# Kernel tuning notes

Hardware: AMD Instinct MI355X
Metric: run time of the kernel (lower is better)

The kernel has to match this reference:

```python
import jax, jax.numpy as jnp
import numpy as np

B, N, D = 2, 2048, 1024
H = 16
HS = D // H
EPS = 1e-6


def layer_norm(x, scale, bias):
    mu = jnp.mean(x, axis=-1, keepdims=True)
    var = jnp.mean(jnp.square(x - mu), axis=-1, keepdims=True)
    return (x - mu) * jax.lax.rsqrt(var + EPS) * scale + bias


def setup_inputs() -> dict:
    key = jax.random.key(0)
    ks = jax.random.split(key, 8)
    lecun = lambda k, shape: jax.random.normal(k, shape, jnp.float32) / jnp.sqrt(shape[0])
    return {
        "x": jax.random.normal(ks[0], (B, N, D), jnp.float32),
        "ln1_scale": jnp.ones((D,), jnp.float32),
        "ln1_bias": jnp.zeros((D,), jnp.float32),
        "w_qkv": lecun(ks[1], (D, 3 * D)),
        "w_out": lecun(ks[2], (D, D)),
        "b_out": jnp.zeros((D,), jnp.float32),
        "ln2_scale": jnp.ones((D,), jnp.float32),
        "ln2_bias": jnp.zeros((D,), jnp.float32),
        "w1": lecun(ks[3], (D, 2 * D)),
        "b1": jnp.zeros((2 * D,), jnp.float32),
        "w2": lecun(ks[4], (2 * D, D)),
        "b2": jnp.zeros((D,), jnp.float32),
    }


def reference(x, ln1_scale, ln1_bias, w_qkv, w_out, b_out,
              ln2_scale, ln2_bias, w1, b1, w2, b2):
    b, n, d = x.shape
    # --- attention sub-block ---
    xn = layer_norm(x, ln1_scale, ln1_bias)
    qkv = xn @ w_qkv                      # [B,N,3D]
    q, k, v = jnp.split(qkv, 3, axis=-1)
    q = q.reshape(b, n, H, HS)
    k = k.reshape(b, n, H, HS)
    v = v.reshape(b, n, H, HS)
    scores = jnp.einsum('bihd,bjhd->bhij', q, k) / jnp.sqrt(jnp.float32(HS))
    causal = jnp.tril(jnp.ones((n, n), bool))[None, None]
    scores = jnp.where(causal, scores, -jnp.inf)
    attn = jax.nn.softmax(scores, axis=-1)
    out_heads = jnp.einsum('bhij,bjhd->bihd', attn, v).reshape(b, n, d)
    x = x + out_heads @ w_out + b_out
    xn2 = layer_norm(x, ln2_scale, ln2_bias)
    y = jax.nn.gelu(xn2 @ w1 + b1)        # flax nn.gelu default approximate=True
    x = x + (y @ w2 + b2)
    return x
```

## Files before the change

### kernel.cpp

```cpp
#include <hip/hip_runtime.h>

#define D_MODEL 1024
#define NSEQ    2048
#define NBATCH  2
#define NHEAD   16
#define HSZ     64
#define MROWS   4096

typedef short s8v  __attribute__((ext_vector_type(8)));
typedef short s4v  __attribute__((ext_vector_type(4)));
typedef float f32x4 __attribute__((ext_vector_type(4)));
typedef float f32x16 __attribute__((ext_vector_type(16)));

#define AS1(p) ((__attribute__((address_space(1))) const void*)(p))
#define AS3(p) ((__attribute__((address_space(3))) void*)(p))

__device__ __forceinline__ float b2f(unsigned short s) {
    union { unsigned u; float f; } z; z.u = (unsigned)s << 16; return z.f;
}
__device__ __forceinline__ unsigned short f2b(float f) {
    union { float f; unsigned u; } z; z.f = f;
    unsigned r = z.u + 0x7fffu + ((z.u >> 16) & 1u);
    return (unsigned short)(r >> 16);
}
__device__ __forceinline__ unsigned short f2b_trunc(float f) {
    union { float f; unsigned u; } z; z.f = f;
    return (unsigned short)(z.u >> 16);
}
__device__ __forceinline__ float gelu_f(float x) {
    float u = 0.7978845608028654f * (x + 0.044715f * x * x * x);
    float t = 1.f - 2.f / (1.f + __expf(2.f * u));
    return 0.5f * x * (1.f + t);
}
__device__ __forceinline__ unsigned cvt_pk_bf16(float lo, float hi) {
    unsigned r;
    asm("v_cvt_pk_bf16_f32 %0, %1, %2" : "=v"(r) : "v"(lo), "v"(hi));
    return r;
}

__global__ __launch_bounds__(256) void sniff_k(const unsigned short* __restrict__ xr,
                                               int* __restrict__ flag) {
    __shared__ int cnt[4];
    int tid = threadIdx.x, ok = 0;
    for (int i = tid; i < 2048; i += 256) {
        unsigned short u = xr[i];
        int e = (u >> 7) & 0xFF;
        if (u == 0 || (e >= 110 && e <= 135)) ok++;
    }
    #pragma unroll
    for (int off = 32; off; off >>= 1) ok += __shfl_down(ok, off);
    if ((tid & 63) == 0) cnt[tid >> 6] = ok;
    __syncthreads();
    if (tid == 0) {
        int tot = cnt[0] + cnt[1] + cnt[2] + cnt[3];
        *flag = (tot > 1843) ? 1 : 0;
    }
}

__global__ __launch_bounds__(256) void cvt_small_k(
    const void* p0, const void* p1, const void* p2, const void* p3,
    const void* p4, const void* p5, const void* p6,
    unsigned short* __restrict__ out, const int* __restrict__ flag)
{
    int i = blockIdx.x * 256 + threadIdx.x;
    const void* src; int off;
    if      (i < 1024) { src = p0; off = i; }
    else if (i < 2048) { src = p1; off = i - 1024; }
    else if (i < 3072) { src = p2; off = i - 2048; }
    else if (i < 4096) { src = p3; off = i - 3072; }
    else if (i < 5120) { src = p4; off = i - 4096; }
    else if (i < 7168) { src = p5; off = i - 5120; }
    else               { src = p6; off = i - 7168; }
    out[i] = (*flag) ? ((const unsigned short*)src)[off]
                     : f2b(((const float*)src)[off]);
}

__global__ __launch_bounds__(256) void transpose_all_k(
    const void* wqkv, const void* wout, const void* w1, const void* w2,
    unsigned short* t_qkv, unsigned short* t_out,
    unsigned short* t_w1, unsigned short* t_w2, const int* __restrict__ flag)
{
    __shared__ unsigned short t[32][33];
    int bid = blockIdx.x;
    const void* W; unsigned short* Wt; int K, N, bx, by;
    if      (bid < 3072) { W = wqkv; Wt = t_qkv; K = 1024; N = 3072; bx = bid % 96; by = bid / 96; }
    else if (bid < 4096) { bid -= 3072; W = wout; Wt = t_out; K = 1024; N = 1024; bx = bid % 32; by = bid / 32; }
    else if (bid < 6144) { bid -= 4096; W = w1;   Wt = t_w1;  K = 1024; N = 2048; bx = bid % 64; by = bid / 64; }
    else                 { bid -= 6144; W = w2;   Wt = t_w2;  K = 2048; N = 1024; bx = bid % 32; by = bid / 32; }
    int f = *flag;
    int n0 = bx * 32, k0 = by * 32;
    int x = threadIdx.x & 31, y = threadIdx.x >> 5;
    #pragma unroll
    for (int r = 0; r < 32; r += 8) {
        size_t idx = (size_t)(k0 + r + y) * N + n0 + x;
        t[r + y][x] = f ? ((const unsigned short*)W)[idx]
                        : f2b(((const float*)W)[idx]);
    }
    __syncthreads();
    #pragma unroll
    for (int r = 0; r < 32; r += 8)
        Wt[(size_t)(n0 + r + y) * K + k0 + x] = t[x][r + y];
}

__global__ __launch_bounds__(256) void ln1f_k(
    const void* __restrict__ x_raw, const unsigned short* __restrict__ scale,
    const unsigned short* __restrict__ bias, unsigned short* __restrict__ xb,
    unsigned short* __restrict__ xn, const int* __restrict__ flag)
{
    int row = blockIdx.x, tid = threadIdx.x;
    int f = *flag;
    float v[4], s = 0.f, s2 = 0.f;
    #pragma unroll
    for (int i = 0; i < 4; ++i) {
        size_t idx = (size_t)row * D_MODEL + tid + i * 256;
        float t = f ? b2f(((const unsigned short*)x_raw)[idx])
                    : ((const float*)x_raw)[idx];
        v[i] = t; s += t; s2 += t * t;
    }
    #pragma unroll
    for (int off = 32; off; off >>= 1) { s += __shfl_down(s, off); s2 += __shfl_down(s2, off); }
    __shared__ float rs[4], rs2[4];
    int w = tid >> 6;
    if ((tid & 63) == 0) { rs[w] = s; rs2[w] = s2; }
    __syncthreads();
    float S  = rs[0] + rs[1] + rs[2] + rs[3];
    float S2 = rs2[0] + rs2[1] + rs2[2] + rs2[3];
    float mean = S * (1.f / D_MODEL);
    float var  = S2 * (1.f / D_MODEL) - mean * mean;
    float rstd = rsqrtf(var + 1e-6f);
    #pragma unroll
    for (int i = 0; i < 4; ++i) {
        int d = tid + i * 256;
        size_t idx = (size_t)row * D_MODEL + d;
        xb[idx] = f2b(v[i]);
        xn[idx] = f2b((v[i] - mean) * rstd * b2f(scale[d]) + b2f(bias[d]));
    }
}

__global__ __launch_bounds__(256) void ln_k(
    const unsigned short* __restrict__ x, const unsigned short* __restrict__ scale,
    const unsigned short* __restrict__ bias, unsigned short* __restrict__ out)
{
    int row = blockIdx.x, tid = threadIdx.x;
    const unsigned short* xr = x + (size_t)row * D_MODEL;
    float v[4], s = 0.f, s2 = 0.f;
    #pragma unroll
    for (int i = 0; i < 4; ++i) {
        float t = b2f(xr[tid + i * 256]);
        v[i] = t; s += t; s2 += t * t;
    }
    #pragma unroll
    for (int off = 32; off; off >>= 1) { s += __shfl_down(s, off); s2 += __shfl_down(s2, off); }
    __shared__ float rs[4], rs2[4];
    int w = tid >> 6;
    if ((tid & 63) == 0) { rs[w] = s; rs2[w] = s2; }
    __syncthreads();
    float S  = rs[0] + rs[1] + rs[2] + rs[3];
    float S2 = rs2[0] + rs2[1] + rs2[2] + rs2[3];
    float mean = S * (1.f / D_MODEL);
    float var  = S2 * (1.f / D_MODEL) - mean * mean;
    float rstd = rsqrtf(var + 1e-6f);
    #pragma unroll
    for (int i = 0; i < 4; ++i) {
        int d = tid + i * 256;
        out[(size_t)row * D_MODEL + d] =
            f2b((v[i] - mean) * rstd * b2f(scale[d]) + b2f(bias[d]));
    }
}

template<int TN, int ACT, int RES, int ODYN>
__global__ __launch_bounds__(256) void gemm128_k(
    const unsigned short* __restrict__ A, const unsigned short* __restrict__ Bt,
    const unsigned short* __restrict__ bias, const unsigned short* __restrict__ resid,
    void* __restrict__ Cp, int M, int Nn, int K, const int* __restrict__ flag)
{
    constexpr int MT = (TN == 128) ? 4 : 2;
    __shared__ short As[128 * 64];
    __shared__ short Bs[TN * 64];
    int tid = threadIdx.x;
    int m0 = blockIdx.y * 128, n0 = blockIdx.x * TN;
    int lane = tid & 63, w = tid >> 6;
    int a_base = (TN == 128) ? (w >> 1) * 64 : w * 32;
    int b_base = (TN == 128) ? (w & 1) * 64 : 0;
    int mm = lane & 15, q = lane >> 4;

    f32x4 zero = {0.f, 0.f, 0.f, 0.f};
    f32x4 acc[MT][4];
    #pragma unroll
    for (int mt = 0; mt < MT; ++mt)
        #pragma unroll
        for (int nt = 0; nt < 4; ++nt) acc[mt][nt] = zero;

    int grow   = lane >> 3;
    int gchunk = ((lane & 7) ^ grow) * 8;
    const unsigned short* Ab = A  + (size_t)(m0 + w * 32 + grow) * K + gchunk;
    const unsigned short* Bb = Bt + (size_t)(n0 + w * (TN / 4) + grow) * K + gchunk;
    int swz = (mm & 7);

    for (int k0 = 0; k0 < K; k0 += 64) {
        __syncthreads();
        #pragma unroll
        for (int s = 0; s < 4; ++s)
            __builtin_amdgcn_global_load_lds(AS1(Ab + k0 + (size_t)(s * 8) * K),
                                             AS3(&As[(w * 32 + s * 8) * 64]), 16, 0, 0);
        #pragma unroll
        for (int s = 0; s < TN / 32; ++s)
            __builtin_amdgcn_global_load_lds(AS1(Bb + k0 + (size_t)(s * 8) * K),
                                             AS3(&Bs[(w * (TN / 4) + s * 8) * 64]), 16, 0, 0);
        __syncthreads();
        #pragma unroll
        for (int kk = 0; kk < 2; ++kk) {
            int col = ((kk * 4 + q) ^ swz) * 8;
            s8v af[MT], bf[4];
            #pragma unroll
            for (int mt = 0; mt < MT; ++mt)
                af[mt] = *(const s8v*)&As[(a_base + mt * 16 + mm) * 64 + col];
            #pragma unroll
            for (int nt = 0; nt < 4; ++nt)
                bf[nt] = *(const s8v*)&Bs[(b_base + nt * 16 + mm) * 64 + col];
            #pragma unroll
            for (int mt = 0; mt < MT; ++mt)
                #pragma unroll
                for (int nt = 0; nt < 4; ++nt)
                    acc[mt][nt] = __builtin_amdgcn_mfma_f32_16x16x32_bf16(
                        af[mt], bf[nt], acc[mt][nt], 0, 0, 0);
        }
    }

    int f = ODYN ? *flag : 1;
    #pragma unroll
    for (int nt = 0; nt < 4; ++nt) {
        int gc = n0 + b_base + nt * 16 + mm;
        float bv = bias ? b2f(bias[gc]) : 0.f;
        #pragma unroll
        for (int mt = 0; mt < MT; ++mt) {
            #pragma unroll
            for (int r = 0; r < 4; ++r) {
                int gr = m0 + a_base + mt * 16 + q * 4 + r;
                float v = acc[mt][nt][r] + bv;
                if (ACT == 1) v = gelu_f(v);
                if (RES == 1) v += b2f(resid[(size_t)gr * Nn + gc]);
                if (f) ((unsigned short*)Cp)[(size_t)gr * Nn + gc] = f2b(v);
                else   ((float*)Cp)[(size_t)gr * Nn + gc] = v;
            }
        }
    }
}

#define SWZG(r) ((((r) >> 3) ^ (r)) & 7)

__global__ __launch_bounds__(256, 4) void fattn_k(
    const unsigned short* __restrict__ qkv, unsigned short* __restrict__ attn_out)
{
    int bh = blockIdx.x;
    int h = bh & (NHEAD - 1), b = bh >> 4;
    int qt = gridDim.y - 1 - blockIdx.y;
    int q0 = qt * 128;
    size_t base = (size_t)b * NSEQ * (3 * D_MODEL);

    __shared__ __align__(16) short Ks[64 * 64];
    __shared__ __align__(16) short Vt[64 * 64];

    int tid = threadIdx.x, lane = tid & 63, w = tid >> 6;
    int ql = lane & 31, hi = lane >> 5;
    int qw0 = q0 + w * 32;
    int gq = qw0 + ql;

    s8v qB[4];
    {
        const unsigned short* qrow = qkv + base + (size_t)gq * (3 * D_MODEL) + h * HSZ;
        #pragma unroll
        for (int ks = 0; ks < 4; ++ks) {
            s8v v = *(const s8v*)(qrow + ks * 16 + hi * 8);
            #pragma unroll
            for (int e = 0; e < 8; ++e) {
                unsigned short u = (unsigned short)v[e];
                if (u & 0x7f80u) u = (unsigned short)(u - 0x0180u);
                v[e] = (short)u;
            }
            qB[ks] = v;
        }
    }

    const unsigned short* kbase = qkv + base + D_MODEL + h * HSZ;
    const unsigned short* vbase = qkv + base + 2 * D_MODEL + h * HSZ;

    int krow = tid >> 2;
    int kc16 = (tid & 3) * 16;
    int km0  = (tid & 3) * 2;
    int kws0 = krow * 64 + (((km0    ) ^ SWZG(krow)) << 3);
    int kws1 = krow * 64 + (((km0 + 1) ^ SWZG(krow)) << 3);
    int kp = tid >> 3;
    int vd = (tid & 7) * 8;

    f32x16 z16;
    #pragma unroll
    for (int i = 0; i < 16; ++i) z16[i] = 0.f;
    f32x16 accA = z16, accB = z16;
    float l_acc = 0.f;

    int nstages = 2 * qt + 2;

    s8v ka, kb, va, vb;
    {
        const unsigned short* kr_ = kbase + (size_t)krow * (3 * D_MODEL) + kc16;
        ka = *(const s8v*)kr_;
        kb = *(const s8v*)(kr_ + 8);
        const unsigned short* vr_ = vbase + (size_t)(2 * kp) * (3 * D_MODEL) + vd;
        va = *(const s8v*)vr_;
        vb = *(const s8v*)(vr_ + 3 * D_MODEL);
    }

    for (int t = 0; t < nstages; ++t) {
        int j0 = t * 64;
        __syncthreads();
        *(s8v*)&Ks[kws0] = ka;
        *(s8v*)&Ks[kws1] = kb;
        #pragma unroll
        for (int e = 0; e < 8; ++e) {
            unsigned pv = (unsigned)(unsigned short)va[e] |
                          ((unsigned)(unsigned short)vb[e] << 16);
            int idx = (vd + e) * 64 + ((((kp >> 2) ^ (tid & 7) ^ e) & 7) << 3)
                      + ((2 * kp) & 7);
            *(unsigned*)&Vt[idx] = pv;
        }
        if (t + 1 < nstages) {
            const unsigned short* kr_ = kbase + (size_t)(j0 + 64 + krow) * (3 * D_MODEL) + kc16;
            ka = *(const s8v*)kr_;
            kb = *(const s8v*)(kr_ + 8);
            const unsigned short* vr_ = vbase + (size_t)(j0 + 64 + 2 * kp) * (3 * D_MODEL) + vd;
            va = *(const s8v*)vr_;
            vb = *(const s8v*)(vr_ + 3 * D_MODEL);
        }
        __syncthreads();

        if (j0 > qw0 + 31) continue;
        int nkt = (j0 + 32 <= qw0 + 31) ? 2 : 1;
        #pragma unroll
        for (int kt = 0; kt < 2; ++kt) {
            if (kt >= nkt) break;
            f32x16 sc = z16;
            __builtin_amdgcn_s_setprio(1);
            #pragma unroll
            for (int ks = 0; ks < 4; ++ks) {
                int key = kt * 32 + ql;
                s8v kf = *(const s8v*)&Ks[key * 64 + (((2 * ks + hi) ^ SWZG(key)) << 3)];
                sc = __builtin_amdgcn_mfma_f32_32x32x16_bf16(kf, qB[ks], sc, 0, 0, 0);
            }
            __builtin_amdgcn_s_setprio(0);
            bool needmask = (j0 + kt * 32 + 31) > qw0;
            #pragma unroll
            for (int r = 0; r < 16; ++r) {
                float p = __expf(sc[r]);
                if (needmask) {
                    int gk = j0 + kt * 32 + (r & 3) + 8 * (r >> 2) + 4 * hi;
                    if (gk > gq) p = 0.f;
                }
                l_acc += p;
                sc[r] = p;
            }
            #pragma unroll
            for (int slot = 0; slot < 2; ++slot) {
                union { unsigned u[4]; s8v v; } pu;
                pu.u[0] = cvt_pk_bf16(sc[slot * 8 + 0], sc[slot * 8 + 1]);
                pu.u[1] = cvt_pk_bf16(sc[slot * 8 + 2], sc[slot * 8 + 3]);
                pu.u[2] = cvt_pk_bf16(sc[slot * 8 + 4], sc[slot * 8 + 5]);
                pu.u[3] = cvt_pk_bf16(sc[slot * 8 + 6], sc[slot * 8 + 7]);
                int g1 = 4 * kt + 2 * slot;
                __builtin_amdgcn_s_setprio(1);
                #pragma unroll
                for (int dt = 0; dt < 2; ++dt) {
                    int dim = dt * 32 + ql;
                    int sw = SWZG(dim);
                    union { s4v hh[2]; s8v v; } vu;
                    vu.hh[0] = *(const s4v*)&Vt[dim * 64 + (((g1    ) ^ sw) << 3) + 4 * hi];
                    vu.hh[1] = *(const s4v*)&Vt[dim * 64 + (((g1 + 1) ^ sw) << 3) + 4 * hi];
                    if (dt == 0)
                        accA = __builtin_amdgcn_mfma_f32_32x32x16_bf16(pu.v, vu.v, accA, 0, 0, 0);
                    else
                        accB = __builtin_amdgcn_mfma_f32_32x32x16_bf16(pu.v, vu.v, accB, 0, 0, 0);
                }
                __builtin_amdgcn_s_setprio(0);
            }
        }
    }

    l_acc += __shfl_xor(l_acc, 32);
    float linv = 1.f / l_acc;
    unsigned short* orow = attn_out + (size_t)b * NSEQ * D_MODEL + h * HSZ;
    #pragma unroll
    for (int r = 0; r < 16; ++r) {
        int cr = (r & 3) + 8 * (r >> 2) + 4 * hi;
        float ri = __shfl(linv, cr);
        size_t ro = (size_t)(qw0 + cr) * D_MODEL;
        orow[ro + ql]      = f2b(accA[r] * ri);
        orow[ro + 32 + ql] = f2b(accB[r] * ri);
    }
}

extern "C" void kernel_launch(void* const* d_in, const int* in_sizes, int n_in,
                              void* d_out, int out_size, void* d_ws, size_t ws_size,
                              hipStream_t stream)
{
    const void* x_raw  = d_in[0];
    const void* ln1s_r = d_in[1];
    const void* ln1b_r = d_in[2];
    const void* wqkv_r = d_in[3];
    const void* wout_r = d_in[4];
    const void* bout_r = d_in[5];
    const void* ln2s_r = d_in[6];
    const void* ln2b_r = d_in[7];
    const void* w1_r   = d_in[8];
    const void* b1_r   = d_in[9];
    const void* w2_r   = d_in[10];
    const void* b2_r   = d_in[11];

    char* ws = (char*)d_ws;
    const size_t MB = 1024 * 1024;
    unsigned short* wt_qkv = (unsigned short*)(ws + 0 * MB);
    unsigned short* wt_out = (unsigned short*)(ws + 6 * MB);
    unsigned short* wt_w1  = (unsigned short*)(ws + 8 * MB);
    unsigned short* wt_w2  = (unsigned short*)(ws + 12 * MB);
    unsigned short* xb     = (unsigned short*)(ws + 16 * MB);
    unsigned short* xn     = (unsigned short*)(ws + 24 * MB);
    unsigned short* qkvb   = (unsigned short*)(ws + 32 * MB);
    unsigned short* x1     = (unsigned short*)(ws + 48 * MB);
    int*            flag   = (int*)           (ws + 56 * MB);
    unsigned short* cbias  = (unsigned short*)(ws + 56 * MB + 1024);
    unsigned short* attnb  = xn;
    unsigned short* xn2    = xn;
    unsigned short* hb     = qkvb;

    unsigned short* c_ln1s = cbias + 0;
    unsigned short* c_ln1b = cbias + 1024;
    unsigned short* c_bout = cbias + 2048;
    unsigned short* c_ln2s = cbias + 3072;
    unsigned short* c_ln2b = cbias + 4096;
    unsigned short* c_b1   = cbias + 5120;
    unsigned short* c_b2   = cbias + 7168;

    sniff_k<<<1, 256, 0, stream>>>((const unsigned short*)x_raw, flag);
    cvt_small_k<<<32, 256, 0, stream>>>(ln1s_r, ln1b_r, bout_r, ln2s_r, ln2b_r,
                                        b1_r, b2_r, cbias, flag);
    transpose_all_k<<<8192, 256, 0, stream>>>(wqkv_r, wout_r, w1_r, w2_r,
                                              wt_qkv, wt_out, wt_w1, wt_w2, flag);
    ln1f_k<<<MROWS, 256, 0, stream>>>(x_raw, c_ln1s, c_ln1b, xb, xn, flag);
    gemm128_k<128, 0, 0, 0><<<dim3(24, 32), 256, 0, stream>>>(
        xn, wt_qkv, nullptr, nullptr, qkvb, MROWS, 3072, 1024, flag);
    fattn_k<<<dim3(NBATCH * NHEAD, NSEQ / 128), 256, 0, stream>>>(qkvb, attnb);
    gemm128_k<64, 0, 1, 0><<<dim3(16, 32), 256, 0, stream>>>(
        attnb, wt_out, c_bout, xb, x1, MROWS, 1024, 1024, flag);
    ln_k<<<MROWS, 256, 0, stream>>>(x1, c_ln2s, c_ln2b, xn2);
    gemm128_k<128, 1, 0, 0><<<dim3(16, 32), 256, 0, stream>>>(
        xn2, wt_w1, c_b1, nullptr, hb, MROWS, 2048, 1024, flag);
    gemm128_k<64, 0, 1, 1><<<dim3(16, 32), 256, 0, stream>>>(
        hb, wt_w2, c_b2, x1, d_out, MROWS, 1024, 2048, flag);
}
```

Measured before the change: 297.2 us.

## Split attention KV range across two wave groups with 64-row query tiles

The attention kernel now uses 64-query tiles, doubling the grid. The block's four waves form two groups that each take alternate 64-key stages, with separate K/V shared buffers. Partial accumulators and row sums are merged through shared memory before normalisation. This is meant to raise parallelism and shorten the longest causal blocks, at the cost of a reduction step, extra shared memory, and per-group global-load imbalance.

```diff
diff --git a/kernel.cpp b/kernel.cpp
--- a/kernel.cpp
+++ b/kernel.cpp
@@ -11,6 +11,7 @@
 typedef short s4v  __attribute__((ext_vector_type(4)));
 typedef float f32x4 __attribute__((ext_vector_type(4)));
 typedef float f32x16 __attribute__((ext_vector_type(16)));
+typedef unsigned long long u64;
 
 #define AS1(p) ((__attribute__((address_space(1))) const void*)(p))
 #define AS3(p) ((__attribute__((address_space(3))) void*)(p))
@@ -22,10 +23,6 @@
     union { float f; unsigned u; } z; z.f = f;
     unsigned r = z.u + 0x7fffu + ((z.u >> 16) & 1u);
     return (unsigned short)(r >> 16);
-}
-__device__ __forceinline__ unsigned short f2b_trunc(float f) {
-    union { float f; unsigned u; } z; z.f = f;
-    return (unsigned short)(z.u >> 16);
 }
 __device__ __forceinline__ float gelu_f(float x) {
     float u = 0.7978845608028654f * (x + 0.044715f * x * x * x);
@@ -255,15 +252,17 @@
     int bh = blockIdx.x;
     int h = bh & (NHEAD - 1), b = bh >> 4;
     int qt = gridDim.y - 1 - blockIdx.y;
-    int q0 = qt * 128;
+    int q0 = qt * 64;
     size_t base = (size_t)b * NSEQ * (3 * D_MODEL);
 
-    __shared__ __align__(16) short Ks[64 * 64];
-    __shared__ __align__(16) short Vt[64 * 64];
-
+    __shared__ __align__(16) short smem[16384];
     int tid = threadIdx.x, lane = tid & 63, w = tid >> 6;
+    int g = w >> 1, wg = w & 1;
+    short* Ksg = &smem[g * 4096];
+    short* Vtg = &smem[8192 + g * 4096];
+
     int ql = lane & 31, hi = lane >> 5;
-    int qw0 = q0 + w * 32;
+    int qw0 = q0 + wg * 32;
     int gq = qw0 + ql;
 
     s8v qB[4];
@@ -285,13 +284,15 @@
     const unsigned short* kbase = qkv + base + D_MODEL + h * HSZ;
     const unsigned short* vbase = qkv + base + 2 * D_MODEL + h * HSZ;
 
-    int krow = tid >> 2;
-    int kc16 = (tid & 3) * 16;
-    int km0  = (tid & 3) * 2;
-    int kws0 = krow * 64 + (((km0    ) ^ SWZG(krow)) << 3);
-    int kws1 = krow * 64 + (((km0 + 1) ^ SWZG(krow)) << 3);
-    int kp = tid >> 3;
-    int vd = (tid & 7) * 8;
+    int tg = tid & 127;
+    int krow = tg >> 1;
+    int kc16 = (tg & 1) * 32;
+    int km0  = (tg & 1) * 4;
+    int swzk = SWZG(krow);
+    int kq  = tg >> 3;
+    int vd0 = (tg & 7) * 8;
+    int vslot = (kq & 1) * 4;
+    int vgg = kq >> 1;
 
     f32x16 z16;
     #pragma unroll
@@ -299,102 +300,137 @@
     f32x16 accA = z16, accB = z16;
     float l_acc = 0.f;
 
-    int nstages = 2 * qt + 2;
-
-    s8v ka, kb, va, vb;
-    {
-        const unsigned short* kr_ = kbase + (size_t)krow * (3 * D_MODEL) + kc16;
-        ka = *(const s8v*)kr_;
-        kb = *(const s8v*)(kr_ + 8);
-        const unsigned short* vr_ = vbase + (size_t)(2 * kp) * (3 * D_MODEL) + vd;
-        va = *(const s8v*)vr_;
-        vb = *(const s8v*)(vr_ + 3 * D_MODEL);
-    }
-
-    for (int t = 0; t < nstages; ++t) {
-        int j0 = t * 64;
+    int npairs = (qt + 2) >> 1;
+    int s = g;
+    bool valid = (s <= qt);
+
+    s8v ka0, ka1, ka2, ka3, va, vb, vc, vd_;
+    if (valid) {
+        const unsigned short* kr_ = kbase + (size_t)(s * 64 + krow) * (3 * D_MODEL) + kc16;
+        ka0 = *(const s8v*)kr_;
+        ka1 = *(const s8v*)(kr_ + 8);
+        ka2 = *(const s8v*)(kr_ + 16);
+        ka3 = *(const s8v*)(kr_ + 24);
+        const unsigned short* vr_ = vbase + (size_t)(s * 64 + 4 * kq) * (3 * D_MODEL) + vd0;
+        va  = *(const s8v*)vr_;
+        vb  = *(const s8v*)(vr_ + 3 * D_MODEL);
+        vc  = *(const s8v*)(vr_ + 6 * D_MODEL);
+        vd_ = *(const s8v*)(vr_ + 9 * D_MODEL);
+    }
+
+    for (int it = 0; it < npairs; ++it) {
+        int j0 = s * 64;
         __syncthreads();
-        *(s8v*)&Ks[kws0] = ka;
-        *(s8v*)&Ks[kws1] = kb;
-        #pragma unroll
-        for (int e = 0; e < 8; ++e) {
-            unsigned pv = (unsigned)(unsigned short)va[e] |
-                          ((unsigned)(unsigned short)vb[e] << 16);
-            int idx = (vd + e) * 64 + ((((kp >> 2) ^ (tid & 7) ^ e) & 7) << 3)
-                      + ((2 * kp) & 7);
-            *(unsigned*)&Vt[idx] = pv;
-        }
-        if (t + 1 < nstages) {
-            const unsigned short* kr_ = kbase + (size_t)(j0 + 64 + krow) * (3 * D_MODEL) + kc16;
-            ka = *(const s8v*)kr_;
-            kb = *(const s8v*)(kr_ + 8);
-            const unsigned short* vr_ = vbase + (size_t)(j0 + 64 + 2 * kp) * (3 * D_MODEL) + vd;
-            va = *(const s8v*)vr_;
-            vb = *(const s8v*)(vr_ + 3 * D_MODEL);
+        if (valid) {
+            *(s8v*)&Ksg[krow * 64 + (((km0 + 0) ^ swzk) << 3)] = ka0;
+            *(s8v*)&Ksg[krow * 64 + (((km0 + 1) ^ swzk) << 3)] = ka1;
+            *(s8v*)&Ksg[krow * 64 + (((km0 + 2) ^ swzk) << 3)] = ka2;
+            *(s8v*)&Ksg[krow * 64 + (((km0 + 3) ^ swzk) << 3)] = ka3;
+            #pragma unroll
+            for (int e = 0; e < 8; ++e) {
+                unsigned plo = (unsigned)(unsigned short)va[e] |
+                               ((unsigned)(unsigned short)vb[e] << 16);
+                unsigned phi = (unsigned)(unsigned short)vc[e] |
+                               ((unsigned)(unsigned short)vd_[e] << 16);
+                int dim = vd0 + e;
+                int col = ((vgg ^ (((tg & 7) ^ e) & 7)) << 3) + vslot;
+                *(u64*)&Vtg[dim * 64 + col] = (u64)plo | ((u64)phi << 32);
+            }
+        }
+        bool valid_n = (s + 2 <= qt);
+        if (valid_n) {
+            const unsigned short* kr_ = kbase + (size_t)((s + 2) * 64 + krow) * (3 * D_MODEL) + kc16;
+            ka0 = *(const s8v*)kr_;
+            ka1 = *(const s8v*)(kr_ + 8);
+            ka2 = *(const s8v*)(kr_ + 16);
+            ka3 = *(const s8v*)(kr_ + 24);
+            const unsigned short* vr_ = vbase + (size_t)((s + 2) * 64 + 4 * kq) * (3 * D_MODEL) + vd0;
+            va  = *(const s8v*)vr_;
+            vb  = *(const s8v*)(vr_ + 3 * D_MODEL);
+            vc  = *(const s8v*)(vr_ + 6 * D_MODEL);
+            vd_ = *(const s8v*)(vr_ + 9 * D_MODEL);
         }
         __syncthreads();
 
-        if (j0 > qw0 + 31) continue;
-        int nkt = (j0 + 32 <= qw0 + 31) ? 2 : 1;
-        #pragma unroll
-        for (int kt = 0; kt < 2; ++kt) {
-            if (kt >= nkt) break;
-            f32x16 sc = z16;
-            __builtin_amdgcn_s_setprio(1);
-            #pragma unroll
-            for (int ks = 0; ks < 4; ++ks) {
-                int key = kt * 32 + ql;
-                s8v kf = *(const s8v*)&Ks[key * 64 + (((2 * ks + hi) ^ SWZG(key)) << 3)];
-                sc = __builtin_amdgcn_mfma_f32_32x32x16_bf16(kf, qB[ks], sc, 0, 0, 0);
-            }
-            __builtin_amdgcn_s_setprio(0);
-            bool needmask = (j0 + kt * 32 + 31) > qw0;
-            #pragma unroll
-            for (int r = 0; r < 16; ++r) {
-                float p = __expf(sc[r]);
-                if (needmask) {
-                    int gk = j0 + kt * 32 + (r & 3) + 8 * (r >> 2) + 4 * hi;
-                    if (gk > gq) p = 0.f;
-                }
-                l_acc += p;
-                sc[r] = p;
-            }
-            #pragma unroll
-            for (int slot = 0; slot < 2; ++slot) {
-                union { unsigned u[4]; s8v v; } pu;
-                pu.u[0] = cvt_pk_bf16(sc[slot * 8 + 0], sc[slot * 8 + 1]);
-                pu.u[1] = cvt_pk_bf16(sc[slot * 8 + 2], sc[slot * 8 + 3]);
-                pu.u[2] = cvt_pk_bf16(sc[slot * 8 + 4], sc[slot * 8 + 5]);
-                pu.u[3] = cvt_pk_bf16(sc[slot * 8 + 6], sc[slot * 8 + 7]);
-                int g1 = 4 * kt + 2 * slot;
+        if (valid) {
+            int nkt = (j0 + 32 <= qw0 + 31) ? 2 : 1;
+            #pragma unroll
+            for (int kt = 0; kt < 2; ++kt) {
+                if (kt >= nkt) break;
+                f32x16 sc = z16;
                 __builtin_amdgcn_s_setprio(1);
                 #pragma unroll
-                for (int dt = 0; dt < 2; ++dt) {
-                    int dim = dt * 32 + ql;
-                    int sw = SWZG(dim);
-                    union { s4v hh[2]; s8v v; } vu;
-                    vu.hh[0] = *(const s4v*)&Vt[dim * 64 + (((g1    ) ^ sw) << 3) + 4 * hi];
-                    vu.hh[1] = *(const s4v*)&Vt[dim * 64 + (((g1 + 1) ^ sw) << 3) + 4 * hi];
-                    if (dt == 0)
-                        accA = __builtin_amdgcn_mfma_f32_32x32x16_bf16(pu.v, vu.v, accA, 0, 0, 0);
-                    else
-                        accB = __builtin_amdgcn_mfma_f32_32x32x16_bf16(pu.v, vu.v, accB, 0, 0, 0);
+                for (int ks = 0; ks < 4; ++ks) {
+                    int key = kt * 32 + ql;
+                    s8v kf = *(const s8v*)&Ksg[key * 64 + (((2 * ks + hi) ^ SWZG(key)) << 3)];
+                    sc = __builtin_amdgcn_mfma_f32_32x32x16_bf16(kf, qB[ks], sc, 0, 0, 0);
                 }
                 __builtin_amdgcn_s_setprio(0);
+                bool needmask = (j0 + kt * 32 + 31) > qw0;
+                #pragma unroll
+                for (int r = 0; r < 16; ++r) {
+                    float p = __expf(sc[r]);
+                    if (needmask) {
+                        int gk = j0 + kt * 32 + (r & 3) + 8 * (r >> 2) + 4 * hi;
+                        if (gk > gq) p = 0.f;
+                    }
+                    l_acc += p;
+                    sc[r] = p;
+                }
+                #pragma unroll
+                for (int slot = 0; slot < 2; ++slot) {
+                    union { unsigned u[4]; s8v v; } pu;
+                    pu.u[0] = cvt_pk_bf16(sc[slot * 8 + 0], sc[slot * 8 + 1]);
+                    pu.u[1] = cvt_pk_bf16(sc[slot * 8 + 2], sc[slot * 8 + 3]);
+                    pu.u[2] = cvt_pk_bf16(sc[slot * 8 + 4], sc[slot * 8 + 5]);
+                    pu.u[3] = cvt_pk_bf16(sc[slot * 8 + 6], sc[slot * 8 + 7]);
+                    int g1 = 4 * kt + 2 * slot;
+                    __builtin_amdgcn_s_setprio(1);
+                    #pragma unroll
+                    for (int dt = 0; dt < 2; ++dt) {
+                        int dim = dt * 32 + ql;
+                        int sw = SWZG(dim);
+                        union { s4v hh[2]; s8v v; } vu;
+                        vu.hh[0] = *(const s4v*)&Vtg[dim * 64 + (((g1    ) ^ sw) << 3) + 4 * hi];
+                        vu.hh[1] = *(const s4v*)&Vtg[dim * 64 + (((g1 + 1) ^ sw) << 3) + 4 * hi];
+                        if (dt == 0)
+                            accA = __builtin_amdgcn_mfma_f32_32x32x16_bf16(pu.v, vu.v, accA, 0, 0, 0);
+                        else
+                            accB = __builtin_amdgcn_mfma_f32_32x32x16_bf16(pu.v, vu.v, accB, 0, 0, 0);
+                    }
+                    __builtin_amdgcn_s_setprio(0);
+                }
             }
         }
-    }
-
-    l_acc += __shfl_xor(l_acc, 32);
-    float linv = 1.f / l_acc;
-    unsigned short* orow = attn_out + (size_t)b * NSEQ * D_MODEL + h * HSZ;
-    #pragma unroll
-    for (int r = 0; r < 16; ++r) {
-        int cr = (r & 3) + 8 * (r >> 2) + 4 * hi;
-        float ri = __shfl(linv, cr);
-        size_t ro = (size_t)(qw0 + cr) * D_MODEL;
-        orow[ro + ql]      = f2b(accA[r] * ri);
-        orow[ro + 32 + ql] = f2b(accB[r] * ri);
+        s += 2; valid = valid_n;
+    }
+
+    __syncthreads();
+    if (g == 1) {
+        float* scr = (float*)smem;
+        int si = (wg * 64 + lane) * 33;
+        #pragma unroll
+        for (int r = 0; r < 16; ++r) { scr[si + r] = accA[r]; scr[si + 16 + r] = accB[r]; }
+        scr[si + 32] = l_acc;
+    }
+    __syncthreads();
+    if (g == 0) {
+        const float* scr = (const float*)smem;
+        int si = (wg * 64 + lane) * 33;
+        #pragma unroll
+        for (int r = 0; r < 16; ++r) { accA[r] += scr[si + r]; accB[r] += scr[si + 16 + r]; }
+        l_acc += scr[si + 32];
+        l_acc += __shfl_xor(l_acc, 32);
+        float linv = 1.f / l_acc;
+        unsigned short* orow = attn_out + (size_t)b * NSEQ * D_MODEL + h * HSZ;
+        #pragma unroll
+        for (int r = 0; r < 16; ++r) {
+            int cr = (r & 3) + 8 * (r >> 2) + 4 * hi;
+            float ri = __shfl(linv, cr);
+            size_t ro = (size_t)(qw0 + cr) * D_MODEL;
+            orow[ro + ql]      = f2b(accA[r] * ri);
+            orow[ro + 32 + ql] = f2b(accB[r] * ri);
+        }
     }
 }
 
@@ -447,7 +483,7 @@
     ln1f_k<<<MROWS, 256, 0, stream>>>(x_raw, c_ln1s, c_ln1b, xb, xn, flag);
     gemm128_k<128, 0, 0, 0><<<dim3(24, 32), 256, 0, stream>>>(
         xn, wt_qkv, nullptr, nullptr, qkvb, MROWS, 3072, 1024, flag);
-    fattn_k<<<dim3(NBATCH * NHEAD, NSEQ / 128), 256, 0, stream>>>(qkvb, attnb);
+    fattn_k<<<dim3(NBATCH * NHEAD, NSEQ / 64), 256, 0, stream>>>(qkvb, attnb);
     gemm128_k<64, 0, 1, 0><<<dim3(16, 32), 256, 0, stream>>>(
         attnb, wt_out, c_bout, xb, x1, MROWS, 1024, 1024, flag);
     ln_k<<<MROWS, 256, 0, stream>>>(x1, c_ln2s, c_ln2b, xn2);
```

Result: slower. 325.4 us (+9.5%).

## Double-buffer attention K/V tiles with direct-to-LDS loads and smaller query tiles

Applied to the files above, without the earlier changes.

The flash-attention kernel now handles 64-query tiles with 128 threads. K and V tiles are double-buffered in shared memory, with one barrier per stage instead of two. K is streamed straight into LDS via global_load_lds with a pre-swizzled source address. V is packed four keys at a time so each lane does a single 8-wide LDS read per MFMA. The aim is to overlap the next tile's loads with the current tile's compute and to trim the wasted causal work. The cost is twice the shared memory per block and more, smaller blocks.

```diff
diff --git a/kernel.cpp b/kernel.cpp
--- a/kernel.cpp
+++ b/kernel.cpp
@@ -8,9 +8,9 @@
 #define MROWS   4096
 
 typedef short s8v  __attribute__((ext_vector_type(8)));
-typedef short s4v  __attribute__((ext_vector_type(4)));
 typedef float f32x4 __attribute__((ext_vector_type(4)));
 typedef float f32x16 __attribute__((ext_vector_type(16)));
+typedef unsigned long long u64;
 
 #define AS1(p) ((__attribute__((address_space(1))) const void*)(p))
 #define AS3(p) ((__attribute__((address_space(3))) void*)(p))
@@ -22,10 +22,6 @@
     union { float f; unsigned u; } z; z.f = f;
     unsigned r = z.u + 0x7fffu + ((z.u >> 16) & 1u);
     return (unsigned short)(r >> 16);
-}
-__device__ __forceinline__ unsigned short f2b_trunc(float f) {
-    union { float f; unsigned u; } z; z.f = f;
-    return (unsigned short)(z.u >> 16);
 }
 __device__ __forceinline__ float gelu_f(float x) {
     float u = 0.7978845608028654f * (x + 0.044715f * x * x * x);
@@ -249,17 +245,17 @@
 
 #define SWZG(r) ((((r) >> 3) ^ (r)) & 7)
 
-__global__ __launch_bounds__(256, 4) void fattn_k(
+__global__ __launch_bounds__(128, 2) void fattn_k(
     const unsigned short* __restrict__ qkv, unsigned short* __restrict__ attn_out)
 {
     int bh = blockIdx.x;
     int h = bh & (NHEAD - 1), b = bh >> 4;
     int qt = gridDim.y - 1 - blockIdx.y;
-    int q0 = qt * 128;
+    int q0 = qt * 64;
     size_t base = (size_t)b * NSEQ * (3 * D_MODEL);
 
-    __shared__ __align__(16) short Ks[64 * 64];
-    __shared__ __align__(16) short Vt[64 * 64];
+    __shared__ __align__(16) short Ks[2][4096];
+    __shared__ __align__(16) short Vt[2][4096];
 
     int tid = threadIdx.x, lane = tid & 63, w = tid >> 6;
     int ql = lane & 31, hi = lane >> 5;
@@ -270,28 +266,27 @@
     {
         const unsigned short* qrow = qkv + base + (size_t)gq * (3 * D_MODEL) + h * HSZ;
         #pragma unroll
-        for (int ks = 0; ks < 4; ++ks) {
-            s8v v = *(const s8v*)(qrow + ks * 16 + hi * 8);
+        for (int dc = 0; dc < 4; ++dc) {
+            s8v v = *(const s8v*)(qrow + dc * 16 + hi * 8);
             #pragma unroll
             for (int e = 0; e < 8; ++e) {
                 unsigned short u = (unsigned short)v[e];
                 if (u & 0x7f80u) u = (unsigned short)(u - 0x0180u);
                 v[e] = (short)u;
             }
-            qB[ks] = v;
+            qB[dc] = v;
         }
     }
 
     const unsigned short* kbase = qkv + base + D_MODEL + h * HSZ;
     const unsigned short* vbase = qkv + base + 2 * D_MODEL + h * HSZ;
 
-    int krow = tid >> 2;
-    int kc16 = (tid & 3) * 16;
-    int km0  = (tid & 3) * 2;
-    int kws0 = krow * 64 + (((km0    ) ^ SWZG(krow)) << 3);
-    int kws1 = krow * 64 + (((km0 + 1) ^ SWZG(krow)) << 3);
-    int kp = tid >> 3;
-    int vd = (tid & 7) * 8;
+    int kln = lane >> 3, kgs = lane & 7;
+    int kq = tid >> 3, vd0 = (tid & 7) * 8;
+    int pgr = 2 * (kq >> 2) + (kq & 1);
+    int pof = 4 * ((kq >> 1) & 1);
+    int swz0 = (((ql >> 3)    ) ^ ql) & 7;
+    int swz1 = (((ql >> 3) + 4) ^ ql) & 7;
 
     f32x16 z16;
     #pragma unroll
@@ -299,53 +294,66 @@
     f32x16 accA = z16, accB = z16;
     float l_acc = 0.f;
 
-    int nstages = 2 * qt + 2;
-
-    s8v ka, kb, va, vb;
+    int nstages = qt + 1;
+    s8v va, vb, vc, vd_;
+
     {
-        const unsigned short* kr_ = kbase + (size_t)krow * (3 * D_MODEL) + kc16;
-        ka = *(const s8v*)kr_;
-        kb = *(const s8v*)(kr_ + 8);
-        const unsigned short* vr_ = vbase + (size_t)(2 * kp) * (3 * D_MODEL) + vd;
-        va = *(const s8v*)vr_;
-        vb = *(const s8v*)(vr_ + 3 * D_MODEL);
-    }
+        #pragma unroll
+        for (int i = 0; i < 4; ++i) {
+            int key  = i * 16 + w * 8 + kln;
+            int gsrc = kgs ^ (((2 * i + w) ^ kln) & 7);
+            __builtin_amdgcn_global_load_lds(
+                AS1(kbase + (size_t)key * (3 * D_MODEL) + gsrc * 8),
+                AS3(&Ks[0][i * 1024 + w * 512]), 16, 0, 0);
+        }
+        const unsigned short* vr = vbase + (size_t)(4 * kq) * (3 * D_MODEL) + vd0;
+        va  = *(const s8v*)vr;
+        vb  = *(const s8v*)(vr + 3 * D_MODEL);
+        vc  = *(const s8v*)(vr + 6 * D_MODEL);
+        vd_ = *(const s8v*)(vr + 9 * D_MODEL);
+        #pragma unroll
+        for (int e = 0; e < 8; ++e) {
+            unsigned plo = (unsigned)(unsigned short)va[e] | ((unsigned)(unsigned short)vb[e] << 16);
+            unsigned phi = (unsigned)(unsigned short)vc[e] | ((unsigned)(unsigned short)vd_[e] << 16);
+            int dim = vd0 + e;
+            *(u64*)&Vt[0][dim * 64 + ((pgr ^ (((tid & 7) ^ e) & 7)) << 3) + pof] =
+                (u64)plo | ((u64)phi << 32);
+        }
+    }
+    __syncthreads();
 
     for (int t = 0; t < nstages; ++t) {
-        int j0 = t * 64;
-        __syncthreads();
-        *(s8v*)&Ks[kws0] = ka;
-        *(s8v*)&Ks[kws1] = kb;
-        #pragma unroll
-        for (int e = 0; e < 8; ++e) {
-            unsigned pv = (unsigned)(unsigned short)va[e] |
-                          ((unsigned)(unsigned short)vb[e] << 16);
-            int idx = (vd + e) * 64 + ((((kp >> 2) ^ (tid & 7) ^ e) & 7) << 3)
-                      + ((2 * kp) & 7);
-            *(unsigned*)&Vt[idx] = pv;
-        }
-        if (t + 1 < nstages) {
-            const unsigned short* kr_ = kbase + (size_t)(j0 + 64 + krow) * (3 * D_MODEL) + kc16;
-            ka = *(const s8v*)kr_;
-            kb = *(const s8v*)(kr_ + 8);
-            const unsigned short* vr_ = vbase + (size_t)(j0 + 64 + 2 * kp) * (3 * D_MODEL) + vd;
-            va = *(const s8v*)vr_;
-            vb = *(const s8v*)(vr_ + 3 * D_MODEL);
-        }
-        __syncthreads();
-
-        if (j0 > qw0 + 31) continue;
+        int cur = t & 1, j0 = t * 64;
+        bool pre = (t + 1 < nstages);
+        if (pre) {
+            int jn = j0 + 64;
+            #pragma unroll
+            for (int i = 0; i < 4; ++i) {
+                int key  = i * 16 + w * 8 + kln;
+                int gsrc = kgs ^ (((2 * i + w) ^ kln) & 7);
+                __builtin_amdgcn_global_load_lds(
+                    AS1(kbase + (size_t)(jn + key) * (3 * D_MODEL) + gsrc * 8),
+                    AS3(&Ks[cur ^ 1][i * 1024 + w * 512]), 16, 0, 0);
+            }
+            const unsigned short* vr = vbase + (size_t)(jn + 4 * kq) * (3 * D_MODEL) + vd0;
+            va  = *(const s8v*)vr;
+            vb  = *(const s8v*)(vr + 3 * D_MODEL);
+            vc  = *(const s8v*)(vr + 6 * D_MODEL);
+            vd_ = *(const s8v*)(vr + 9 * D_MODEL);
+        }
+        __builtin_amdgcn_sched_barrier(0);
+
         int nkt = (j0 + 32 <= qw0 + 31) ? 2 : 1;
         #pragma unroll
         for (int kt = 0; kt < 2; ++kt) {
             if (kt >= nkt) break;
+            int swzk = kt ? swz1 : swz0;
             f32x16 sc = z16;
             __builtin_amdgcn_s_setprio(1);
             #pragma unroll
-            for (int ks = 0; ks < 4; ++ks) {
-                int key = kt * 32 + ql;
-                s8v kf = *(const s8v*)&Ks[key * 64 + (((2 * ks + hi) ^ SWZG(key)) << 3)];
-                sc = __builtin_amdgcn_mfma_f32_32x32x16_bf16(kf, qB[ks], sc, 0, 0, 0);
+            for (int dc = 0; dc < 4; ++dc) {
+                s8v kf = *(const s8v*)&Ks[cur][(kt * 32 + ql) * 64 + (((2 * dc + hi) ^ swzk) << 3)];
+                sc = __builtin_amdgcn_mfma_f32_32x32x16_bf16(kf, qB[dc], sc, 0, 0, 0);
             }
             __builtin_amdgcn_s_setprio(0);
             bool needmask = (j0 + kt * 32 + 31) > qw0;
@@ -360,29 +368,37 @@
                 sc[r] = p;
             }
             #pragma unroll
-            for (int slot = 0; slot < 2; ++slot) {
+            for (int half = 0; half < 2; ++half) {
                 union { unsigned u[4]; s8v v; } pu;
-                pu.u[0] = cvt_pk_bf16(sc[slot * 8 + 0], sc[slot * 8 + 1]);
-                pu.u[1] = cvt_pk_bf16(sc[slot * 8 + 2], sc[slot * 8 + 3]);
-                pu.u[2] = cvt_pk_bf16(sc[slot * 8 + 4], sc[slot * 8 + 5]);
-                pu.u[3] = cvt_pk_bf16(sc[slot * 8 + 6], sc[slot * 8 + 7]);
-                int g1 = 4 * kt + 2 * slot;
+                pu.u[0] = cvt_pk_bf16(sc[half * 8 + 0], sc[half * 8 + 1]);
+                pu.u[1] = cvt_pk_bf16(sc[half * 8 + 2], sc[half * 8 + 3]);
+                pu.u[2] = cvt_pk_bf16(sc[half * 8 + 4], sc[half * 8 + 5]);
+                pu.u[3] = cvt_pk_bf16(sc[half * 8 + 6], sc[half * 8 + 7]);
+                int gb = 4 * kt + 2 * half + hi;
                 __builtin_amdgcn_s_setprio(1);
-                #pragma unroll
-                for (int dt = 0; dt < 2; ++dt) {
-                    int dim = dt * 32 + ql;
-                    int sw = SWZG(dim);
-                    union { s4v hh[2]; s8v v; } vu;
-                    vu.hh[0] = *(const s4v*)&Vt[dim * 64 + (((g1    ) ^ sw) << 3) + 4 * hi];
-                    vu.hh[1] = *(const s4v*)&Vt[dim * 64 + (((g1 + 1) ^ sw) << 3) + 4 * hi];
-                    if (dt == 0)
-                        accA = __builtin_amdgcn_mfma_f32_32x32x16_bf16(pu.v, vu.v, accA, 0, 0, 0);
-                    else
-                        accB = __builtin_amdgcn_mfma_f32_32x32x16_bf16(pu.v, vu.v, accB, 0, 0, 0);
+                {
+                    s8v vv = *(const s8v*)&Vt[cur][ql * 64 + ((gb ^ swz0) << 3)];
+                    accA = __builtin_amdgcn_mfma_f32_32x32x16_bf16(pu.v, vv, accA, 0, 0, 0);
+                }
+                {
+                    s8v vv = *(const s8v*)&Vt[cur][(32 + ql) * 64 + ((gb ^ swz1) << 3)];
+                    accB = __builtin_amdgcn_mfma_f32_32x32x16_bf16(pu.v, vv, accB, 0, 0, 0);
                 }
                 __builtin_amdgcn_s_setprio(0);
             }
         }
+
+        if (pre) {
+            #pragma unroll
+            for (int e = 0; e < 8; ++e) {
+                unsigned plo = (unsigned)(unsigned short)va[e] | ((unsigned)(unsigned short)vb[e] << 16);
+                unsigned phi = (unsigned)(unsigned short)vc[e] | ((unsigned)(unsigned short)vd_[e] << 16);
+                int dim = vd0 + e;
+                *(u64*)&Vt[cur ^ 1][dim * 64 + ((pgr ^ (((tid & 7) ^ e) & 7)) << 3) + pof] =
+                    (u64)plo | ((u64)phi << 32);
+            }
+        }
+        __syncthreads();
     }
 
     l_acc += __shfl_xor(l_acc, 32);
@@ -447,7 +463,7 @@
     ln1f_k<<<MROWS, 256, 0, stream>>>(x_raw, c_ln1s, c_ln1b, xb, xn, flag);
     gemm128_k<128, 0, 0, 0><<<dim3(24, 32), 256, 0, stream>>>(
         xn, wt_qkv, nullptr, nullptr, qkvb, MROWS, 3072, 1024, flag);
-    fattn_k<<<dim3(NBATCH * NHEAD, NSEQ / 128), 256, 0, stream>>>(qkvb, attnb);
+    fattn_k<<<dim3(NBATCH * NHEAD, NSEQ / 64), 128, 0, stream>>>(qkvb, attnb);
     gemm128_k<64, 0, 1, 0><<<dim3(16, 32), 256, 0, stream>>>(
         attnb, wt_out, c_bout, xb, x1, MROWS, 1024, 1024, flag);
     ln_k<<<MROWS, 256, 0, stream>>>(x1, c_ln2s, c_ln2b, xn2);
```

Measured after the change: 309.6 us. 1.04x slower.
